# Kernel optimization log

Hardware: AMD Instinct MI355X
Metric: run time of the kernel (lower is better)

The kernel has to match this reference:

```python
import jax, jax.numpy as jnp
import numpy as np

B, S, HIDDEN = 2, 2048, 2048
N_HEADS, N_KV_HEADS = 32, 8
HEAD_DIM = HIDDEN // N_HEADS          # 64
HALF = HEAD_DIM // 2                  # 32
N_REP = N_HEADS // N_KV_HEADS         # 4
NEG_INF = -1e9


def setup_inputs() -> dict:
    key = jax.random.key(0)
    ks = jax.random.split(key, 5)
    scale = 0.02
    x = jax.random.normal(ks[0], (B, S, HIDDEN), dtype=jnp.float32)
    wq = jax.random.normal(ks[1], (HIDDEN, N_HEADS * HEAD_DIM), dtype=jnp.float32) * scale
    wk = jax.random.normal(ks[2], (HIDDEN, N_KV_HEADS * HEAD_DIM), dtype=jnp.float32) * scale
    wv = jax.random.normal(ks[3], (HIDDEN, N_KV_HEADS * HEAD_DIM), dtype=jnp.float32) * scale
    wo = jax.random.normal(ks[4], (HIDDEN, HIDDEN), dtype=jnp.float32) * scale
    # Llama rotary frequencies: theta = 10000^{-2i/d}, angles = pos * theta
    inv_freq = 1.0 / (10000.0 ** (np.arange(0, HEAD_DIM, 2, dtype=np.float32) / HEAD_DIM))
    angles = np.arange(S, dtype=np.float32)[:, None] * inv_freq[None, :]  # [S, HALF]
    freqs_cos = jnp.asarray(np.cos(angles), dtype=jnp.float32)
    freqs_sin = jnp.asarray(np.sin(angles), dtype=jnp.float32)
    mask = jnp.tril(jnp.ones((S, S), dtype=bool))[None, None]  # causal [1,1,S,S]
    return {"x": x, "wq": wq, "wk": wk, "wv": wv, "wo": wo,
            "freqs_cos": freqs_cos, "freqs_sin": freqs_sin, "mask": mask}


def _apply_rope(t, cos, sin):
    # t: [B, S, H, HEAD_DIM]; cos/sin: [S, HALF] -> broadcast [1, S, 1, HALF]
    tr, ti = t[..., ::2], t[..., 1::2]           # real/imag halves (interleaved pairing)
    c = cos[None, :, None, :]
    s = sin[None, :, None, :]
    out_r = tr * c - ti * s
    out_i = tr * s + ti * c
    out = jnp.stack([out_r, out_i], axis=-1)     # [B,S,H,HALF,2]
    return out.reshape(t.shape)                  # re-interleave


def reference(x, wq, wk, wv, wo, freqs_cos, freqs_sin, mask):
    b, s, _ = x.shape
    xq = (x @ wq).reshape(b, s, N_HEADS, HEAD_DIM)
    xk = (x @ wk).reshape(b, s, N_KV_HEADS, HEAD_DIM)
    xv = (x @ wv).reshape(b, s, N_KV_HEADS, HEAD_DIM)
    xq = _apply_rope(xq, freqs_cos, freqs_sin)
    xk = _apply_rope(xk, freqs_cos, freqs_sin)
    # repeat_kv: interleave-repeat kv heads to match query heads
    xk = jnp.repeat(xk, N_REP, axis=2)           # [B,S,N_HEADS,HEAD_DIM]
    xv = jnp.repeat(xv, N_REP, axis=2)
    q = jnp.transpose(xq, (0, 2, 1, 3))          # [B,H,S,D]
    k = jnp.transpose(xk, (0, 2, 1, 3))
    v = jnp.transpose(xv, (0, 2, 1, 3))
    attn = jnp.einsum('bhqd,bhkd->bhqk', q, k) / jnp.sqrt(jnp.float32(HEAD_DIM))
    attn = attn + (1.0 - mask.astype(attn.dtype)) * NEG_INF  # keras Softmax masking
    attn = jax.nn.softmax(attn, axis=-1)
    out = jnp.einsum('bhqk,bhkd->bhqd', attn, v)
    out = jnp.transpose(out, (0, 2, 1, 3)).reshape(b, s, HIDDEN)
    return out @ wo
```

## Files before the change

kernel.cpp:

```cpp
#include <hip/hip_runtime.h>
#include <cstdint>
#include <cstddef>

#define S_LEN 2048
#define HIDDEN 2048
#define NH 32
#define NKV 8
#define HD 64
#define QKV_W 3072

typedef __bf16 bf16;
typedef __bf16 bf16x8 __attribute__((ext_vector_type(8)));
typedef __bf16 bf16x4 __attribute__((ext_vector_type(4)));
typedef float f32x4 __attribute__((ext_vector_type(4)));

__device__ __forceinline__ void async16(const bf16* g, bf16* l) {
  __builtin_amdgcn_global_load_lds((const __attribute__((address_space(1))) void*)g,
                                   (__attribute__((address_space(3))) void*)l, 16, 0, 0);
}

__device__ __forceinline__ int swz8(int row, int col) {
  return (((col >> 3) ^ (row & 7)) << 3) | (col & 7);
}

__global__ void cast_x_kernel(const float* __restrict__ in, bf16* __restrict__ out, int n4) {
  int i = blockIdx.x * blockDim.x + threadIdx.x;
  if (i >= n4) return;
  f32x4 v = ((const f32x4*)in)[i];
  bf16x4 o;
  o[0] = (bf16)v[0]; o[1] = (bf16)v[1]; o[2] = (bf16)v[2]; o[3] = (bf16)v[3];
  ((bf16x4*)out)[i] = o;
}

__global__ void transpose_cast_kernel(const float* __restrict__ in, bf16* __restrict__ out,
                                      int K, int N) {
  __shared__ float tile[32][33];
  const int n0 = blockIdx.x * 32, k0 = blockIdx.y * 32;
  const int tx = threadIdx.x, ty = threadIdx.y;
#pragma unroll
  for (int i = 0; i < 32; i += 8)
    tile[ty + i][tx] = in[(size_t)(k0 + ty + i) * N + n0 + tx];
  __syncthreads();
#pragma unroll
  for (int i = 0; i < 32; i += 8)
    out[(size_t)(n0 + ty + i) * K + k0 + tx] = (bf16)tile[tx][ty + i];
}

__global__ void vt_kernel(const bf16* __restrict__ qkv, bf16* __restrict__ vt) {
  __shared__ bf16 tile[32][33];
  const int s0 = blockIdx.x * 32, c0 = blockIdx.y * 32, b = blockIdx.z;
  const int tx = threadIdx.x, ty = threadIdx.y;
#pragma unroll
  for (int i = 0; i < 32; i += 8)
    tile[ty + i][tx] = qkv[((size_t)b * S_LEN + s0 + ty + i) * QKV_W + 2560 + c0 + tx];
  __syncthreads();
#pragma unroll
  for (int i = 0; i < 32; i += 8)
    vt[((size_t)b * 512 + c0 + ty + i) * S_LEN + s0 + tx] = tile[tx][ty + i];
}

template <int OUT_BF16>
__global__ __launch_bounds__(256) void gemm_bt_kernel(const bf16* __restrict__ A,
                                                      const bf16* __restrict__ Bt,
                                                      void* __restrict__ Cv,
                                                      int M, int N, int K) {
  __shared__ bf16 Al[128 * 32];
  __shared__ bf16 Bl[128 * 32];
  const int tid = threadIdx.x;
  const int lane = tid & 63, w = tid >> 6;
  const int quad = lane >> 4, l16 = lane & 15;
  const int m0 = blockIdx.y * 128, n0 = blockIdx.x * 128;
  const int wm = (w >> 1) * 64, wn = (w & 1) * 64;
  f32x4 acc[4][4] = {};
  const int srow = tid >> 2, scol = (tid & 3) * 8;
  const bf16* Ar0 = A + (size_t)(m0 + srow) * K + scol;
  const bf16* Ar1 = A + (size_t)(m0 + 64 + srow) * K + scol;
  const bf16* Br0 = Bt + (size_t)(n0 + srow) * K + scol;
  const bf16* Br1 = Bt + (size_t)(n0 + 64 + srow) * K + scol;
  bf16* al0 = Al + tid * 8;
  bf16* al1 = Al + 2048 + tid * 8;
  bf16* bl0 = Bl + tid * 8;
  bf16* bl1 = Bl + 2048 + tid * 8;
  for (int kt = 0; kt < K; kt += 32) {
    __syncthreads();
    async16(Ar0 + kt, al0);
    async16(Ar1 + kt, al1);
    async16(Br0 + kt, bl0);
    async16(Br1 + kt, bl1);
    __syncthreads();
    bf16x8 a[4], b[4];
#pragma unroll
    for (int mi = 0; mi < 4; ++mi)
      a[mi] = *(const bf16x8*)(Al + (wm + mi * 16 + l16) * 32 + quad * 8);
#pragma unroll
    for (int ni = 0; ni < 4; ++ni)
      b[ni] = *(const bf16x8*)(Bl + (wn + ni * 16 + l16) * 32 + quad * 8);
#pragma unroll
    for (int mi = 0; mi < 4; ++mi)
#pragma unroll
      for (int ni = 0; ni < 4; ++ni)
        acc[mi][ni] = __builtin_amdgcn_mfma_f32_16x16x32_bf16(a[mi], b[ni], acc[mi][ni], 0, 0, 0);
  }
#pragma unroll
  for (int mi = 0; mi < 4; ++mi)
#pragma unroll
    for (int ni = 0; ni < 4; ++ni)
#pragma unroll
      for (int i = 0; i < 4; ++i) {
        const int row = m0 + wm + mi * 16 + quad * 4 + i;
        const int col = n0 + wn + ni * 16 + l16;
        if (OUT_BF16)
          ((bf16*)Cv)[(size_t)row * N + col] = (bf16)acc[mi][ni][i];
        else
          ((float*)Cv)[(size_t)row * N + col] = acc[mi][ni][i];
      }
}

__global__ void rope_kernel(bf16* __restrict__ qkv, const float* __restrict__ cosp,
                            const float* __restrict__ sinp, int total) {
  int idx = blockIdx.x * blockDim.x + threadIdx.x;
  if (idx >= total) return;
  const int row = idx / 320;
  const int col = (idx - row * 320) * 8;
  const int s = row & (S_LEN - 1);
  const int j0 = (col >> 1) & 31;
  bf16* ptr = qkv + (size_t)row * QKV_W + col;
  bf16x8 v = *(bf16x8*)ptr;
#pragma unroll
  for (int u = 0; u < 4; ++u) {
    const float tr = (float)v[2 * u], ti = (float)v[2 * u + 1];
    const float c = cosp[s * 32 + j0 + u], sn = sinp[s * 32 + j0 + u];
    v[2 * u] = (bf16)(tr * c - ti * sn);
    v[2 * u + 1] = (bf16)(tr * sn + ti * c);
  }
  *(bf16x8*)ptr = v;
}

__global__ __launch_bounds__(256) void attn_kernel(const bf16* __restrict__ qkv,
                                                   const bf16* __restrict__ vt,
                                                   bf16* __restrict__ out) {
  __shared__ bf16 Kl[64 * 64];
  __shared__ bf16 Vl[64 * 64];
  __shared__ bf16 Pl[4][16 * 64];
  const int tid = threadIdx.x;
  const int lane = tid & 63, w = tid >> 6;
  const int quad = lane >> 4, l16 = lane & 15;
  int id = blockIdx.x;
  const int kvh = id & 7; id >>= 3;
  const int gx = id & 15; id >>= 4;
  const int rep = id & 3; const int b = id >> 2;
  const int h = kvh * 4 + rep;
  const bf16* Qbase = qkv + ((size_t)b * S_LEN) * QKV_W + h * HD;
  const bf16* Kbase = qkv + ((size_t)b * S_LEN) * QKV_W + 2048 + kvh * HD;
  const bf16* Vtb = vt + ((size_t)b * 512 + kvh * 64) * S_LEN;
  const int srow = tid >> 3;
  const int gcol = ((tid & 7) ^ (srow & 7)) * 8;
  const bf16* Ksrc0 = Kbase + (size_t)srow * QKV_W + gcol;
  const bf16* Ksrc1 = Kbase + (size_t)(srow + 32) * QKV_W + gcol;
  const bf16* Vsrc0 = Vtb + (size_t)srow * S_LEN + gcol;
  const bf16* Vsrc1 = Vtb + (size_t)(srow + 32) * S_LEN + gcol;

  for (int pass = 0; pass < 2; ++pass) {
    const int qt = pass ? (31 - gx) : gx;
    const int q0 = qt * 64;
    const int qrow = q0 + w * 16 + l16;
    const bf16x8 aq0 = *(const bf16x8*)(Qbase + (size_t)qrow * QKV_W + quad * 8);
    const bf16x8 aq1 = *(const bf16x8*)(Qbase + (size_t)qrow * QKV_W + 32 + quad * 8);
    float lsum = 0.f;
    f32x4 o[4] = {};

    for (int t = 0; t <= qt; ++t) {
      const int kt = t * 64;
      __syncthreads();
      async16(Ksrc0 + (size_t)kt * QKV_W, Kl + tid * 8);
      async16(Ksrc1 + (size_t)kt * QKV_W, Kl + 2048 + tid * 8);
      async16(Vsrc0 + kt, Vl + tid * 8);
      async16(Vsrc1 + kt, Vl + 2048 + tid * 8);
      __syncthreads();
      f32x4 c[4] = {};
#pragma unroll
      for (int j = 0; j < 4; ++j) {
        const int kr = j * 16 + l16;
        const bf16x8 bk0 = *(const bf16x8*)&Kl[kr * 64 + swz8(kr, quad * 8)];
        const bf16x8 bk1 = *(const bf16x8*)&Kl[kr * 64 + swz8(kr, 32 + quad * 8)];
        c[j] = __builtin_amdgcn_mfma_f32_16x16x32_bf16(bk0, aq0, c[j], 0, 0, 0);
        c[j] = __builtin_amdgcn_mfma_f32_16x16x32_bf16(bk1, aq1, c[j], 0, 0, 0);
      }
      float p[4][4];
#pragma unroll
      for (int j = 0; j < 4; ++j)
#pragma unroll
        for (int i = 0; i < 4; ++i)
          p[j][i] = exp2f(fmaf(c[j][i], 0.18033688f, -5.7707801f));
      if (t == qt) {
        const int qrel = w * 16 + l16;
#pragma unroll
        for (int j = 0; j < 4; ++j)
#pragma unroll
          for (int i = 0; i < 4; ++i)
            if (j * 16 + quad * 4 + i > qrel) p[j][i] = 0.f;
      }
#pragma unroll
      for (int j = 0; j < 4; ++j) {
        lsum += (p[j][0] + p[j][1]) + (p[j][2] + p[j][3]);
        bf16x4 pv;
        pv[0] = (bf16)p[j][0]; pv[1] = (bf16)p[j][1];
        pv[2] = (bf16)p[j][2]; pv[3] = (bf16)p[j][3];
        *(bf16x4*)&Pl[w][l16 * 64 + swz8(l16, j * 16 + quad * 4)] = pv;
      }
      const bf16x8 ap0 = *(const bf16x8*)&Pl[w][l16 * 64 + swz8(l16, quad * 8)];
      const bf16x8 ap1 = *(const bf16x8*)&Pl[w][l16 * 64 + swz8(l16, 32 + quad * 8)];
#pragma unroll
      for (int dt = 0; dt < 4; ++dt) {
        const int vr = dt * 16 + l16;
        const bf16x8 bv0 = *(const bf16x8*)&Vl[vr * 64 + swz8(vr, quad * 8)];
        const bf16x8 bv1 = *(const bf16x8*)&Vl[vr * 64 + swz8(vr, 32 + quad * 8)];
        o[dt] = __builtin_amdgcn_mfma_f32_16x16x32_bf16(ap0, bv0, o[dt], 0, 0, 0);
        o[dt] = __builtin_amdgcn_mfma_f32_16x16x32_bf16(ap1, bv1, o[dt], 0, 0, 0);
      }
    }
    float ls = lsum;
    ls += __shfl_xor(ls, 16);
    ls += __shfl_xor(ls, 32);
    const float rlq = 1.0f / ls;
#pragma unroll
    for (int i = 0; i < 4; ++i) {
      const float rl = __shfl(rlq, (lane & 48) | (quad * 4 + i));
      const int r = q0 + w * 16 + quad * 4 + i;
#pragma unroll
      for (int dt = 0; dt < 4; ++dt)
        out[((size_t)b * S_LEN + r) * HIDDEN + h * HD + dt * 16 + l16] = (bf16)(o[dt][i] * rl);
    }
  }
}

extern "C" void kernel_launch(void* const* d_in, const int* in_sizes, int n_in,
                              void* d_out, int out_size, void* d_ws, size_t ws_size,
                              hipStream_t stream) {
  const float* x = (const float*)d_in[0];
  const float* wq = (const float*)d_in[1];
  const float* wk = (const float*)d_in[2];
  const float* wv = (const float*)d_in[3];
  const float* wo = (const float*)d_in[4];
  const float* fc = (const float*)d_in[5];
  const float* fs = (const float*)d_in[6];

  char* ws = (char*)d_ws;
  bf16* xb   = (bf16*)(ws);
  bf16* wT   = (bf16*)(ws + 16777216);
  bf16* woT  = (bf16*)(ws + 29360128);
  bf16* qkv  = (bf16*)(ws + 37748736);
  bf16* aout = (bf16*)(ws + 62914560);
  bf16* vt   = xb;

  cast_x_kernel<<<8192, 256, 0, stream>>>(x, xb, 2097152);
  transpose_cast_kernel<<<dim3(64, 64), dim3(32, 8), 0, stream>>>(wq, wT, 2048, 2048);
  transpose_cast_kernel<<<dim3(16, 64), dim3(32, 8), 0, stream>>>(wk, wT + (size_t)2048 * 2048, 2048, 512);
  transpose_cast_kernel<<<dim3(16, 64), dim3(32, 8), 0, stream>>>(wv, wT + (size_t)2560 * 2048, 2048, 512);
  transpose_cast_kernel<<<dim3(64, 64), dim3(32, 8), 0, stream>>>(wo, woT, 2048, 2048);

  gemm_bt_kernel<1><<<dim3(24, 32), 256, 0, stream>>>(xb, wT, (void*)qkv, 4096, 3072, 2048);
  rope_kernel<<<5120, 256, 0, stream>>>(qkv, fc, fs, 1310720);
  vt_kernel<<<dim3(64, 16, 2), dim3(32, 8), 0, stream>>>(qkv, vt);
  attn_kernel<<<1024, 256, 0, stream>>>(qkv, vt, aout);
  gemm_bt_kernel<0><<<dim3(16, 32), 256, 0, stream>>>(aout, woT, d_out, 4096, 2048, 2048);
}
```

Measured before the change: 353.8 us.

## Double attention query tile to 128 rows per block to reuse K/V tiles

Each warp now processes two 16-row query groups (32 rows), so a block covers 128 query rows and each loaded K/V tile feeds twice as many MFMAs. The grid halves to 512 blocks with paired causal passes, and per-group causal skipping avoids work for query groups whose keys lie entirely in the masked region. This reduces global K/V traffic and barrier overhead per unit of compute. In exchange it uses more registers and LDS, and with fewer blocks the GPU may be less well occupied or less evenly balanced.

Result: no change. 349.0 us (-1.3%).

```diff
diff --git a/kernel.cpp b/kernel.cpp
--- a/kernel.cpp
+++ b/kernel.cpp
@@ -141,13 +141,13 @@
                                                    bf16* __restrict__ out) {
   __shared__ bf16 Kl[64 * 64];
   __shared__ bf16 Vl[64 * 64];
-  __shared__ bf16 Pl[4][16 * 64];
+  __shared__ bf16 Pl[4][32 * 64];
   const int tid = threadIdx.x;
   const int lane = tid & 63, w = tid >> 6;
   const int quad = lane >> 4, l16 = lane & 15;
   int id = blockIdx.x;
   const int kvh = id & 7; id >>= 3;
-  const int gx = id & 15; id >>= 4;
+  const int gx = id & 7; id >>= 3;
   const int rep = id & 3; const int b = id >> 2;
   const int h = kvh * 4 + rep;
   const bf16* Qbase = qkv + ((size_t)b * S_LEN) * QKV_W + h * HD;
@@ -161,15 +161,20 @@
   const bf16* Vsrc1 = Vtb + (size_t)(srow + 32) * S_LEN + gcol;
 
   for (int pass = 0; pass < 2; ++pass) {
-    const int qt = pass ? (31 - gx) : gx;
-    const int q0 = qt * 64;
-    const int qrow = q0 + w * 16 + l16;
-    const bf16x8 aq0 = *(const bf16x8*)(Qbase + (size_t)qrow * QKV_W + quad * 8);
-    const bf16x8 aq1 = *(const bf16x8*)(Qbase + (size_t)qrow * QKV_W + 32 + quad * 8);
-    float lsum = 0.f;
-    f32x4 o[4] = {};
-
-    for (int t = 0; t <= qt; ++t) {
+    const int qt = pass ? (15 - gx) : gx;
+    const int qbase = qt * 128 + w * 32;
+    bf16x8 aq[2][2];
+#pragma unroll
+    for (int g = 0; g < 2; ++g) {
+      const size_t qr = (size_t)(qbase + g * 16 + l16) * QKV_W;
+      aq[g][0] = *(const bf16x8*)(Qbase + qr + quad * 8);
+      aq[g][1] = *(const bf16x8*)(Qbase + qr + 32 + quad * 8);
+    }
+    float lsum0 = 0.f, lsum1 = 0.f;
+    f32x4 o[2][4] = {};
+
+    const int nt = 2 * qt + 2;
+    for (int t = 0; t < nt; ++t) {
       const int kt = t * 64;
       __syncthreads();
       async16(Ksrc0 + (size_t)kt * QKV_W, Kl + tid * 8);
@@ -177,59 +182,90 @@
       async16(Vsrc0 + kt, Vl + tid * 8);
       async16(Vsrc1 + kt, Vl + 2048 + tid * 8);
       __syncthreads();
-      f32x4 c[4] = {};
+      const bool on0 = kt <= qbase + 15;
+      const bool on1 = kt <= qbase + 31;
+      if (!on1) continue;
+      f32x4 c[2][4] = {};
 #pragma unroll
       for (int j = 0; j < 4; ++j) {
         const int kr = j * 16 + l16;
         const bf16x8 bk0 = *(const bf16x8*)&Kl[kr * 64 + swz8(kr, quad * 8)];
         const bf16x8 bk1 = *(const bf16x8*)&Kl[kr * 64 + swz8(kr, 32 + quad * 8)];
-        c[j] = __builtin_amdgcn_mfma_f32_16x16x32_bf16(bk0, aq0, c[j], 0, 0, 0);
-        c[j] = __builtin_amdgcn_mfma_f32_16x16x32_bf16(bk1, aq1, c[j], 0, 0, 0);
-      }
-      float p[4][4];
-#pragma unroll
-      for (int j = 0; j < 4; ++j)
-#pragma unroll
-        for (int i = 0; i < 4; ++i)
-          p[j][i] = exp2f(fmaf(c[j][i], 0.18033688f, -5.7707801f));
-      if (t == qt) {
-        const int qrel = w * 16 + l16;
+        c[1][j] = __builtin_amdgcn_mfma_f32_16x16x32_bf16(bk0, aq[1][0], c[1][j], 0, 0, 0);
+        c[1][j] = __builtin_amdgcn_mfma_f32_16x16x32_bf16(bk1, aq[1][1], c[1][j], 0, 0, 0);
+        if (on0) {
+          c[0][j] = __builtin_amdgcn_mfma_f32_16x16x32_bf16(bk0, aq[0][0], c[0][j], 0, 0, 0);
+          c[0][j] = __builtin_amdgcn_mfma_f32_16x16x32_bf16(bk1, aq[0][1], c[0][j], 0, 0, 0);
+        }
+      }
+#pragma unroll
+      for (int g = 0; g < 2; ++g) {
+        if (!(g ? on1 : on0)) continue;
+        const int qrow = qbase + g * 16;
+        float p[4][4];
 #pragma unroll
         for (int j = 0; j < 4; ++j)
 #pragma unroll
           for (int i = 0; i < 4; ++i)
-            if (j * 16 + quad * 4 + i > qrel) p[j][i] = 0.f;
-      }
-#pragma unroll
-      for (int j = 0; j < 4; ++j) {
-        lsum += (p[j][0] + p[j][1]) + (p[j][2] + p[j][3]);
-        bf16x4 pv;
-        pv[0] = (bf16)p[j][0]; pv[1] = (bf16)p[j][1];
-        pv[2] = (bf16)p[j][2]; pv[3] = (bf16)p[j][3];
-        *(bf16x4*)&Pl[w][l16 * 64 + swz8(l16, j * 16 + quad * 4)] = pv;
-      }
-      const bf16x8 ap0 = *(const bf16x8*)&Pl[w][l16 * 64 + swz8(l16, quad * 8)];
-      const bf16x8 ap1 = *(const bf16x8*)&Pl[w][l16 * 64 + swz8(l16, 32 + quad * 8)];
+            p[j][i] = exp2f(fmaf(c[g][j][i], 0.18033688f, -5.7707801f));
+        if (kt + 63 > qrow) {
+          const int qabs = qrow + l16;
+#pragma unroll
+          for (int j = 0; j < 4; ++j)
+#pragma unroll
+            for (int i = 0; i < 4; ++i)
+              if (kt + j * 16 + quad * 4 + i > qabs) p[j][i] = 0.f;
+        }
+        float ls = 0.f;
+#pragma unroll
+        for (int j = 0; j < 4; ++j) {
+          ls += (p[j][0] + p[j][1]) + (p[j][2] + p[j][3]);
+          bf16x4 pv;
+          pv[0] = (bf16)p[j][0]; pv[1] = (bf16)p[j][1];
+          pv[2] = (bf16)p[j][2]; pv[3] = (bf16)p[j][3];
+          const int pr = g * 16 + l16;
+          *(bf16x4*)&Pl[w][pr * 64 + swz8(pr, j * 16 + quad * 4)] = pv;
+        }
+        if (g) lsum1 += ls; else lsum0 += ls;
+      }
+      bf16x8 ap0l, ap0h, ap1l, ap1h;
+      {
+        const int pr1 = 16 + l16;
+        ap1l = *(const bf16x8*)&Pl[w][pr1 * 64 + swz8(pr1, quad * 8)];
+        ap1h = *(const bf16x8*)&Pl[w][pr1 * 64 + swz8(pr1, 32 + quad * 8)];
+        if (on0) {
+          ap0l = *(const bf16x8*)&Pl[w][l16 * 64 + swz8(l16, quad * 8)];
+          ap0h = *(const bf16x8*)&Pl[w][l16 * 64 + swz8(l16, 32 + quad * 8)];
+        }
+      }
 #pragma unroll
       for (int dt = 0; dt < 4; ++dt) {
         const int vr = dt * 16 + l16;
         const bf16x8 bv0 = *(const bf16x8*)&Vl[vr * 64 + swz8(vr, quad * 8)];
         const bf16x8 bv1 = *(const bf16x8*)&Vl[vr * 64 + swz8(vr, 32 + quad * 8)];
-        o[dt] = __builtin_amdgcn_mfma_f32_16x16x32_bf16(ap0, bv0, o[dt], 0, 0, 0);
-        o[dt] = __builtin_amdgcn_mfma_f32_16x16x32_bf16(ap1, bv1, o[dt], 0, 0, 0);
+        o[1][dt] = __builtin_amdgcn_mfma_f32_16x16x32_bf16(ap1l, bv0, o[1][dt], 0, 0, 0);
+        o[1][dt] = __builtin_amdgcn_mfma_f32_16x16x32_bf16(ap1h, bv1, o[1][dt], 0, 0, 0);
+        if (on0) {
+          o[0][dt] = __builtin_amdgcn_mfma_f32_16x16x32_bf16(ap0l, bv0, o[0][dt], 0, 0, 0);
+          o[0][dt] = __builtin_amdgcn_mfma_f32_16x16x32_bf16(ap0h, bv1, o[0][dt], 0, 0, 0);
+        }
       }
     }
-    float ls = lsum;
-    ls += __shfl_xor(ls, 16);
-    ls += __shfl_xor(ls, 32);
-    const float rlq = 1.0f / ls;
-#pragma unroll
-    for (int i = 0; i < 4; ++i) {
-      const float rl = __shfl(rlq, (lane & 48) | (quad * 4 + i));
-      const int r = q0 + w * 16 + quad * 4 + i;
-#pragma unroll
-      for (int dt = 0; dt < 4; ++dt)
-        out[((size_t)b * S_LEN + r) * HIDDEN + h * HD + dt * 16 + l16] = (bf16)(o[dt][i] * rl);
+#pragma unroll
+    for (int g = 0; g < 2; ++g) {
+      float ls = g ? lsum1 : lsum0;
+      ls += __shfl_xor(ls, 16);
+      ls += __shfl_xor(ls, 32);
+      const float rlq = 1.0f / ls;
+#pragma unroll
+      for (int i = 0; i < 4; ++i) {
+        const float rl = __shfl(rlq, (lane & 48) | (quad * 4 + i));
+        const int r = qbase + g * 16 + quad * 4 + i;
+#pragma unroll
+        for (int dt = 0; dt < 4; ++dt)
+          out[((size_t)b * S_LEN + r) * HIDDEN + h * HD + dt * 16 + l16] =
+              (bf16)(o[g][dt][i] * rl);
+      }
     }
   }
 }
@@ -262,6 +298,6 @@
   gemm_bt_kernel<1><<<dim3(24, 32), 256, 0, stream>>>(xb, wT, (void*)qkv, 4096, 3072, 2048);
   rope_kernel<<<5120, 256, 0, stream>>>(qkv, fc, fs, 1310720);
   vt_kernel<<<dim3(64, 16, 2), dim3(32, 8), 0, stream>>>(qkv, vt);
-  attn_kernel<<<1024, 256, 0, stream>>>(qkv, vt, aout);
+  attn_kernel<<<512, 256, 0, stream>>>(qkv, vt, aout);
   gemm_bt_kernel<0><<<dim3(16, 32), 256, 0, stream>>>(aout, woT, d_out, 4096, 2048, 2048);
 }
```
